# Kernel tuning notes

Measured on AMD Instinct MI355X. Metric: run time of the kernel, lower is better.

Reference implementation:

```python
import jax, jax.numpy as jnp
import numpy as np
from jax import lax

NEGINF = -100000.0
START_IDX = 0  # y_codebook['__START__']
TAGSET = 16


def setup_inputs() -> dict:
    key = jax.random.key(0)
    ks = jax.random.split(key, 8)
    D, H, K, T = 1024, 1024, TAGSET, 8192
    seq = jax.random.normal(ks[0], (1, T, D), dtype=jnp.float32)
    # PyTorch-layout LSTM params: gates ordered (i, f, g, o)
    s = 1.0 / np.sqrt(H)
    W_ih = jax.random.uniform(ks[1], (4 * H, D), jnp.float32, -s, s)
    W_hh = jax.random.uniform(ks[2], (4 * H, H), jnp.float32, -s, s)
    b_ih = jax.random.uniform(ks[3], (4 * H,), jnp.float32, -s, s)
    b_hh = jax.random.uniform(ks[4], (4 * H,), jnp.float32, -s, s)
    W_tag = jax.random.uniform(ks[5], (K, H), jnp.float32, -s, s)
    b_tag = jax.random.uniform(ks[6], (K,), jnp.float32, -s, s)
    trans = jax.random.normal(ks[7], (K, K), dtype=jnp.float32)
    trans = trans.at[:, START_IDX].set(NEGINF)  # nothing transitions INTO start
    return {"seq": seq, "W_ih": W_ih, "W_hh": W_hh, "b_ih": b_ih,
            "b_hh": b_hh, "W_tag": W_tag, "b_tag": b_tag, "trans": trans}


def _lstm(x, W_ih, W_hh, b_ih, b_hh):
    # x: (T, D) -> hidden states (T, H); PyTorch gate order i,f,g,o
    H = W_hh.shape[1]
    x_gates = x @ W_ih.T + (b_ih + b_hh)  # (T, 4H) precomputed input part

    def step(carry, gx):
        h, c = carry
        g = gx + h @ W_hh.T
        i, f, gg, o = jnp.split(g, 4)
        i, f, o = jax.nn.sigmoid(i), jax.nn.sigmoid(f), jax.nn.sigmoid(o)
        c = f * c + i * jnp.tanh(gg)
        h = o * jnp.tanh(c)
        return (h, c), h

    init = (jnp.zeros((H,), x.dtype), jnp.zeros((H,), x.dtype))
    _, hs = lax.scan(step, init, x_gates)
    return hs  # (T, H)


def reference(seq, W_ih, W_hh, b_ih, b_hh, W_tag, b_tag, trans):
    # --- compute_potential (batch=1) ---
    x = seq[0]                                  # (T, D)
    rnnout = _lstm(x, W_ih, W_hh, b_ih, b_hh)    # (T, H)
    feat = rnnout @ W_tag.T + b_tag              # (T, K) unary potentials

    # --- compute_forward_vec: alpha recursion in log-semiring ---
    # feat_score[t, i, j] = feat[t, j] + trans[i, j]
    feat_score = feat[:, None, :] + trans[None, :, :]  # (T, K, K)
    K = trans.shape[0]
    alpha0 = jnp.full((K,), NEGINF, dtype=feat.dtype).at[START_IDX].set(0.0)

    def step(a, fs):
        a_new = jax.nn.logsumexp(a[:, None] + fs, axis=0)  # (K,)
        return a_new, a_new

    a_T, rows = lax.scan(step, alpha0, feat_score)
    alpha = jnp.concatenate([alpha0[None, :], rows], axis=0)  # (T+1, K)
    Z = jax.nn.logsumexp(a_T)  # log partition (no stop state)
    return Z, alpha
```

## Files before the change

### kernel.cpp

```cpp
#include <hip/hip_runtime.h>
#include <hip/hip_bf16.h>
#include <math.h>

#define T_LEN   8192
#define D_IN    1024
#define H_DIM   1024
#define G4      4096
#define K_TAG   16
#define NWG     128
#define NPAIR   512
#define NC      128
#define CLEN    64
#define NEGINF_V (-100000.0f)

__device__ __forceinline__ float fsig(float x) {
  return __fdividef(1.f, 1.f + __expf(-x));
}
__device__ __forceinline__ float ftanh(float x) {
  float e = __expf(fminf(fmaxf(2.f * x, -88.f), 88.f));
  return __fdividef(e - 1.f, e + 1.f);
}

__global__ void k_init(const float* __restrict__ b_ih, const float* __restrict__ b_hh,
                       float* __restrict__ bsum, float* __restrict__ h0,
                       unsigned long long* __restrict__ htag) {
  int tid = blockIdx.x * 256 + threadIdx.x;
  if (tid < G4) bsum[tid] = b_ih[tid] + b_hh[tid];
  if (tid < H_DIM) h0[tid] = 0.f;
  if (tid < 2 * NPAIR) htag[tid] = 0ULL;
}

__global__ __launch_bounds__(256) void k_gemm_xg(
    const float* __restrict__ A,
    const float* __restrict__ B,
    const float* __restrict__ bsum,
    __hip_bfloat16* __restrict__ xg)
{
  __shared__ __align__(16) float As[16][132];
  __shared__ __align__(16) float Bs[16][132];
  const int tid = threadIdx.x;
  const int n0 = blockIdx.x * 128;
  const int m0 = blockIdx.y * 128;
  const int ty = tid >> 4, tx = tid & 15;
  float acc[8][8] = {};

  for (int k0 = 0; k0 < D_IN; k0 += 16) {
#pragma unroll
    for (int p0 = 0; p0 < 2; ++p0) {
      int p = tid + p0 * 256;
      int row = p >> 2;
      int c4 = (p & 3) * 4;
      float4 va = *(const float4*)&A[(size_t)(m0 + row) * D_IN + k0 + c4];
      As[c4 + 0][row] = va.x; As[c4 + 1][row] = va.y;
      As[c4 + 2][row] = va.z; As[c4 + 3][row] = va.w;
      float4 vb = *(const float4*)&B[(size_t)(n0 + row) * D_IN + k0 + c4];
      Bs[c4 + 0][row] = vb.x; Bs[c4 + 1][row] = vb.y;
      Bs[c4 + 2][row] = vb.z; Bs[c4 + 3][row] = vb.w;
    }
    __syncthreads();
#pragma unroll
    for (int k = 0; k < 16; ++k) {
      float4 a0 = *(const float4*)&As[k][ty * 8];
      float4 a1 = *(const float4*)&As[k][ty * 8 + 4];
      float4 b0 = *(const float4*)&Bs[k][tx * 8];
      float4 b1 = *(const float4*)&Bs[k][tx * 8 + 4];
      float av[8] = {a0.x, a0.y, a0.z, a0.w, a1.x, a1.y, a1.z, a1.w};
      float bv[8] = {b0.x, b0.y, b0.z, b0.w, b1.x, b1.y, b1.z, b1.w};
#pragma unroll
      for (int i = 0; i < 8; ++i)
#pragma unroll
        for (int j = 0; j < 8; ++j)
          acc[i][j] = fmaf(av[i], bv[j], acc[i][j]);
    }
    __syncthreads();
  }

#pragma unroll
  for (int i = 0; i < 8; ++i) {
    size_t m = (size_t)(m0 + ty * 8 + i);
    union { __hip_bfloat16 h[8]; uint4 v; } pk;
#pragma unroll
    for (int j = 0; j < 8; ++j)
      pk.h[j] = __float2bfloat16(acc[i][j] + bsum[n0 + tx * 8 + j]);
    *(uint4*)&xg[m * G4 + n0 + tx * 8] = pk.v;
  }
}

__global__ __launch_bounds__(256) void k_lstm(
    const float* __restrict__ W_hh,
    const __hip_bfloat16* __restrict__ xg,
    float* __restrict__ h_all,
    unsigned long long* __restrict__ htag)
{
  __shared__ __align__(16) float h_lds[H_DIM];
  __shared__ unsigned long long hxs[4];

  const int tid = threadIdx.x;
  const int w = blockIdx.x;
  const int lane = tid & 63;
  const int v = tid >> 6;
  const int rl8 = lane >> 3;
  const int sub = lane & 7;
  const int g = rl8 >> 1, b = rl8 & 1;
  const int j = 2 * v + b;
  const int grow = g * H_DIM + w * 8 + j;

  float4 w4[32];
#pragma unroll
  for (int k = 0; k < 32; ++k)
    w4[k] = *(const float4*)&W_hh[(size_t)grow * H_DIM + sub * 4 + 32 * k];

  if (tid < 4) hxs[tid] = 0ULL;
  __syncthreads();

  float c_reg = 0.f;

  for (int t = 1; t <= T_LEN; ++t) {
    float xgv = __bfloat162float(xg[(size_t)(t - 1) * G4 + grow]);

    if (v == 0) {
      unsigned long long* hb = htag + (((t - 1) & 1) << 9);
      const unsigned tgt = (unsigned)(t - 1);
      unsigned long long x0, x1, x2, x3, x4, x5, x6, x7;
      for (;;) {
        x0 = __hip_atomic_load(hb + lane,       __ATOMIC_RELAXED, __HIP_MEMORY_SCOPE_AGENT);
        x1 = __hip_atomic_load(hb + lane + 64,  __ATOMIC_RELAXED, __HIP_MEMORY_SCOPE_AGENT);
        x2 = __hip_atomic_load(hb + lane + 128, __ATOMIC_RELAXED, __HIP_MEMORY_SCOPE_AGENT);
        x3 = __hip_atomic_load(hb + lane + 192, __ATOMIC_RELAXED, __HIP_MEMORY_SCOPE_AGENT);
        x4 = __hip_atomic_load(hb + lane + 256, __ATOMIC_RELAXED, __HIP_MEMORY_SCOPE_AGENT);
        x5 = __hip_atomic_load(hb + lane + 320, __ATOMIC_RELAXED, __HIP_MEMORY_SCOPE_AGENT);
        x6 = __hip_atomic_load(hb + lane + 384, __ATOMIC_RELAXED, __HIP_MEMORY_SCOPE_AGENT);
        x7 = __hip_atomic_load(hb + lane + 448, __ATOMIC_RELAXED, __HIP_MEMORY_SCOPE_AGENT);
        unsigned mn = min(min(min((unsigned)(x0 >> 32), (unsigned)(x1 >> 32)),
                              min((unsigned)(x2 >> 32), (unsigned)(x3 >> 32))),
                          min(min((unsigned)(x4 >> 32), (unsigned)(x5 >> 32)),
                              min((unsigned)(x6 >> 32), (unsigned)(x7 >> 32))));
        if (mn >= tgt) break;
        __builtin_amdgcn_s_sleep(1);
      }
      unsigned long long xs[8] = {x0, x1, x2, x3, x4, x5, x6, x7};
#pragma unroll
      for (int i = 0; i < 8; ++i) {
        unsigned lo = (unsigned)xs[i];
        unsigned short s0 = (unsigned short)lo;
        unsigned short s1 = (unsigned short)(lo >> 16);
        float2 p;
        p.x = __bfloat162float(*(const __hip_bfloat16*)&s0);
        p.y = __bfloat162float(*(const __hip_bfloat16*)&s1);
        ((float2*)h_lds)[lane + 64 * i] = p;
      }
    }
    __syncthreads();

    const float4* h4 = (const float4*)h_lds;
    float acc = 0.f;
#pragma unroll
    for (int k = 0; k < 32; ++k) {
      float4 hv = h4[sub + 8 * k];
      acc = fmaf(w4[k].x, hv.x, acc);
      acc = fmaf(w4[k].y, hv.y, acc);
      acc = fmaf(w4[k].z, hv.z, acc);
      acc = fmaf(w4[k].w, hv.w, acc);
    }
    acc += __shfl_xor(acc, 1);
    acc += __shfl_xor(acc, 2);
    acc += __shfl_xor(acc, 4);
    acc += xgv;

    const int bl = lane & 8;
    float gi = __shfl(acc, bl);
    float gf = __shfl(acc, bl | 16);
    float gg = __shfl(acc, bl | 32);
    float go = __shfl(acc, bl | 48);

    float si = fsig(gi);
    float sf = fsig(gf);
    float so = fsig(go);
    c_reg = sf * c_reg + si * ftanh(gg);
    float h = so * ftanh(c_reg);
    float h_other = __shfl(h, lane ^ 8);

    if (lane == 0) {
      __hip_bfloat16 hb0 = __float2bfloat16(h);
      __hip_bfloat16 hb1 = __float2bfloat16(h_other);
      unsigned lo = (unsigned)*(unsigned short*)&hb0 |
                    ((unsigned)*(unsigned short*)&hb1 << 16);
      unsigned long long pk = ((unsigned long long)(unsigned)t << 32) |
                              (unsigned long long)lo;
      __hip_atomic_store(&hxs[v], pk, __ATOMIC_RELAXED, __HIP_MEMORY_SCOPE_WORKGROUP);
    }
    if ((lane & 55) == 0) {
      h_all[(size_t)t * H_DIM + w * 8 + j] = h;
    }

    if (v == 0 && lane < 4) {
      unsigned long long pk;
      do {
        pk = __hip_atomic_load(&hxs[lane], __ATOMIC_RELAXED, __HIP_MEMORY_SCOPE_WORKGROUP);
      } while ((unsigned)(pk >> 32) != (unsigned)t);
      __hip_atomic_store(htag + ((t & 1) << 9) + w * 4 + lane, pk,
                         __ATOMIC_RELAXED, __HIP_MEMORY_SCOPE_AGENT);
    }
  }
}

__device__ __forceinline__ float lse16(float v) {
  float m = v;
  m = fmaxf(m, __shfl_xor(m, 1));
  m = fmaxf(m, __shfl_xor(m, 2));
  m = fmaxf(m, __shfl_xor(m, 4));
  m = fmaxf(m, __shfl_xor(m, 8));
  float e = expf(v - m);
  e += __shfl_xor(e, 1);
  e += __shfl_xor(e, 2);
  e += __shfl_xor(e, 4);
  e += __shfl_xor(e, 8);
  return m + logf(e);
}

__global__ __launch_bounds__(256) void k_chunk(
    const float* __restrict__ h_all,
    const float* __restrict__ W_tag, const float* __restrict__ b_tag,
    const float* __restrict__ trans,
    float* __restrict__ featbuf,
    float* __restrict__ Pbuf)
{
  __shared__ float trs[16][17];
  __shared__ float featc[CLEN][16];
  __shared__ __align__(16) float hrow[H_DIM];
  __shared__ float red[16][17];
  __shared__ float Pa[16][17], Pb[16][17];

  const int tid = threadIdx.x;
  const int c = blockIdx.x;
  trs[tid >> 4][tid & 15] = trans[tid];

  const int jj = tid & 15, part = tid >> 4;
  for (int u = 0; u < CLEN; ++u) {
    int s = c * CLEN + 1 + u;
    ((float4*)hrow)[tid] = ((const float4*)(h_all + (size_t)s * H_DIM))[tid];
    __syncthreads();
    const float* wt = W_tag + (size_t)jj * H_DIM + part * 64;
    const float* hp = hrow + part * 64;
    float4 a4 = {0.f, 0.f, 0.f, 0.f};
#pragma unroll
    for (int k2 = 0; k2 < 64; k2 += 4) {
      float4 hv = *(const float4*)(hp + k2);
      float4 wv = *(const float4*)(wt + k2);
      a4.x = fmaf(hv.x, wv.x, a4.x);
      a4.y = fmaf(hv.y, wv.y, a4.y);
      a4.z = fmaf(hv.z, wv.z, a4.z);
      a4.w = fmaf(hv.w, wv.w, a4.w);
    }
    red[jj][part] = (a4.x + a4.y) + (a4.z + a4.w);
    __syncthreads();
    if (tid < 16) {
      float ssum = b_tag[tid];
#pragma unroll
      for (int pp = 0; pp < 16; ++pp) ssum += red[tid][pp];
      featc[u][tid] = ssum;
      featbuf[(size_t)s * K_TAG + tid] = ssum;
    }
    __syncthreads();
  }

  const int i = tid >> 4, j = tid & 15;
  Pa[i][j] = trs[i][j] + featc[0][j];
  __syncthreads();
  float* Pr = &Pa[0][0];
  float* Pw = &Pb[0][0];
  for (int u = 1; u < CLEN; ++u) {
    float fj = featc[u][j];
    float m = -3.0e38f;
#pragma unroll
    for (int k = 0; k < 16; ++k) m = fmaxf(m, Pr[i * 17 + k] + trs[k][j]);
    float e = 0.f;
#pragma unroll
    for (int k = 0; k < 16; ++k) e += expf(Pr[i * 17 + k] + trs[k][j] - m);
    Pw[i * 17 + j] = m + fj + logf(e);
    __syncthreads();
    float* tsw = Pr; Pr = Pw; Pw = tsw;
  }
  Pbuf[(size_t)c * 256 + i * 16 + j] = Pr[i * 17 + j];
}

__global__ __launch_bounds__(256) void k_scan(
    const float* __restrict__ Pbuf,
    float* __restrict__ bbuf,
    float* __restrict__ out)
{
  __shared__ float Pl[16][17];
  __shared__ float bcur[16], bnew[16];
  const int tid = threadIdx.x;
  const int i = tid & 15, j = tid >> 4;
  if (tid < 16) {
    float a0 = (tid == 0) ? 0.f : NEGINF_V;
    bcur[tid] = a0;
    bbuf[tid] = a0;
    out[1 + tid] = a0;
  }
  __syncthreads();
  for (int c = 0; c < NC; ++c) {
    Pl[tid >> 4][tid & 15] = Pbuf[(size_t)c * 256 + tid];
    __syncthreads();
    float r_ = lse16(bcur[i] + Pl[i][j]);
    if (i == 0) bnew[j] = r_;
    __syncthreads();
    if (tid < 16) {
      bcur[tid] = bnew[tid];
      bbuf[(size_t)(c + 1) * K_TAG + tid] = bnew[tid];
    }
    __syncthreads();
  }
  if (tid < 16) {
    float z = lse16(bcur[tid]);
    if (tid == 0) out[0] = z;
  }
}

__global__ __launch_bounds__(256) void k_alpha(
    const float* __restrict__ featbuf, const float* __restrict__ trans,
    const float* __restrict__ bbuf, float* __restrict__ out)
{
  __shared__ float trs[16][17];
  __shared__ float acur[16], anew[16];
  const int tid = threadIdx.x;
  const int c = blockIdx.x;
  trs[tid >> 4][tid & 15] = trans[tid];
  if (tid < 16) acur[tid] = bbuf[(size_t)c * K_TAG + tid];
  __syncthreads();
  const int i = tid & 15, j = tid >> 4;
  for (int u = 0; u < CLEN; ++u) {
    int s = c * CLEN + 1 + u;
    float v = acur[i] + trs[i][j] + featbuf[(size_t)s * K_TAG + j];
    float r_ = lse16(v);
    if (i == 0) anew[j] = r_;
    __syncthreads();
    if (tid < 16) {
      acur[tid] = anew[tid];
      out[1 + (size_t)s * K_TAG + tid] = anew[tid];
    }
    __syncthreads();
  }
}

extern "C" void kernel_launch(void* const* d_in, const int* in_sizes, int n_in,
                              void* d_out, int out_size, void* d_ws, size_t ws_size,
                              hipStream_t stream) {
  (void)in_sizes; (void)n_in; (void)out_size; (void)ws_size;
  const float* seq   = (const float*)d_in[0];
  const float* W_ih  = (const float*)d_in[1];
  const float* W_hh  = (const float*)d_in[2];
  const float* b_ih  = (const float*)d_in[3];
  const float* b_hh  = (const float*)d_in[4];
  const float* W_tag = (const float*)d_in[5];
  const float* b_tag = (const float*)d_in[6];
  const float* trans = (const float*)d_in[7];
  float* out = (float*)d_out;

  char* base = (char*)d_ws;
  size_t off = 0;
  auto take = [&](size_t nbytes) -> void* {
    void* p = base + off;
    off += (nbytes + 255) & ~(size_t)255;
    return p;
  };
  __hip_bfloat16* xg = (__hip_bfloat16*)take((size_t)T_LEN * G4 * sizeof(__hip_bfloat16));
  float* h_all   = (float*)take((size_t)(T_LEN + 1) * H_DIM * sizeof(float));
  float* featbuf = (float*)take((size_t)(T_LEN + 1) * K_TAG * sizeof(float));
  float* Pbuf    = (float*)take((size_t)NC * 256 * sizeof(float));
  float* bbuf    = (float*)take((size_t)(NC + 1) * K_TAG * sizeof(float));
  float* bsum    = (float*)take((size_t)G4 * sizeof(float));
  unsigned long long* htag = (unsigned long long*)take((size_t)2 * NPAIR * sizeof(unsigned long long));

  k_init<<<16, 256, 0, stream>>>(b_ih, b_hh, bsum, h_all, htag);
  k_gemm_xg<<<dim3(G4 / 128, T_LEN / 128), 256, 0, stream>>>(seq, W_ih, bsum, xg);
  k_lstm<<<NWG, 256, 0, stream>>>(W_hh, xg, h_all, htag);
  k_chunk<<<NC, 256, 0, stream>>>(h_all, W_tag, b_tag, trans, featbuf, Pbuf);
  k_scan<<<1, 256, 0, stream>>>(Pbuf, bbuf, out);
  k_alpha<<<NC, 256, 0, stream>>>(featbuf, trans, bbuf, out);
}
```

Before: 20.07 ms.

## Halve persistent LSTM workgroups to 64 with 512 threads and split FMA chains

The persistent recurrent LSTM kernel now runs 64 workgroups of 512 threads, each owning 16 hidden units instead of 8, so fewer workgroups take part in the per-step cross-workgroup flag exchange. The goal is to cut global synchronisation latency per timestep. The dot product also now uses four independent accumulators to shorten the serial FMA dependency chain. In exchange, each workgroup does more work per step, register pressure under the 512-thread launch bound may rise, and only half as many compute units are used.

```diff
diff --git a/kernel.cpp b/kernel.cpp
--- a/kernel.cpp
+++ b/kernel.cpp
@@ -7,7 +7,7 @@
 #define H_DIM   1024
 #define G4      4096
 #define K_TAG   16
-#define NWG     128
+#define NWG     64
 #define NPAIR   512
 #define NC      128
 #define CLEN    64
@@ -86,14 +86,14 @@
   }
 }
 
-__global__ __launch_bounds__(256) void k_lstm(
+__global__ __launch_bounds__(512) void k_lstm(
     const float* __restrict__ W_hh,
     const __hip_bfloat16* __restrict__ xg,
     float* __restrict__ h_all,
     unsigned long long* __restrict__ htag)
 {
   __shared__ __align__(16) float h_lds[H_DIM];
-  __shared__ unsigned long long hxs[4];
+  __shared__ unsigned long long hxs[8];
 
   const int tid = threadIdx.x;
   const int w = blockIdx.x;
@@ -103,14 +103,14 @@
   const int sub = lane & 7;
   const int g = rl8 >> 1, b = rl8 & 1;
   const int j = 2 * v + b;
-  const int grow = g * H_DIM + w * 8 + j;
+  const int grow = g * H_DIM + w * 16 + j;
 
   float4 w4[32];
 #pragma unroll
   for (int k = 0; k < 32; ++k)
     w4[k] = *(const float4*)&W_hh[(size_t)grow * H_DIM + sub * 4 + 32 * k];
 
-  if (tid < 4) hxs[tid] = 0ULL;
+  if (tid < 8) hxs[tid] = 0ULL;
   __syncthreads();
 
   float c_reg = 0.f;
@@ -153,15 +153,31 @@
     __syncthreads();
 
     const float4* h4 = (const float4*)h_lds;
-    float acc = 0.f;
-#pragma unroll
-    for (int k = 0; k < 32; ++k) {
-      float4 hv = h4[sub + 8 * k];
-      acc = fmaf(w4[k].x, hv.x, acc);
-      acc = fmaf(w4[k].y, hv.y, acc);
-      acc = fmaf(w4[k].z, hv.z, acc);
-      acc = fmaf(w4[k].w, hv.w, acc);
-    }
+    float ac0 = 0.f, ac1 = 0.f, ac2 = 0.f, ac3 = 0.f;
+#pragma unroll
+    for (int k = 0; k < 32; k += 4) {
+      float4 hv0 = h4[sub + 8 * k];
+      float4 hv1 = h4[sub + 8 * (k + 1)];
+      float4 hv2 = h4[sub + 8 * (k + 2)];
+      float4 hv3 = h4[sub + 8 * (k + 3)];
+      ac0 = fmaf(w4[k].x, hv0.x, ac0);
+      ac0 = fmaf(w4[k].y, hv0.y, ac0);
+      ac0 = fmaf(w4[k].z, hv0.z, ac0);
+      ac0 = fmaf(w4[k].w, hv0.w, ac0);
+      ac1 = fmaf(w4[k + 1].x, hv1.x, ac1);
+      ac1 = fmaf(w4[k + 1].y, hv1.y, ac1);
+      ac1 = fmaf(w4[k + 1].z, hv1.z, ac1);
+      ac1 = fmaf(w4[k + 1].w, hv1.w, ac1);
+      ac2 = fmaf(w4[k + 2].x, hv2.x, ac2);
+      ac2 = fmaf(w4[k + 2].y, hv2.y, ac2);
+      ac2 = fmaf(w4[k + 2].z, hv2.z, ac2);
+      ac2 = fmaf(w4[k + 2].w, hv2.w, ac2);
+      ac3 = fmaf(w4[k + 3].x, hv3.x, ac3);
+      ac3 = fmaf(w4[k + 3].y, hv3.y, ac3);
+      ac3 = fmaf(w4[k + 3].z, hv3.z, ac3);
+      ac3 = fmaf(w4[k + 3].w, hv3.w, ac3);
+    }
+    float acc = (ac0 + ac1) + (ac2 + ac3);
     acc += __shfl_xor(acc, 1);
     acc += __shfl_xor(acc, 2);
     acc += __shfl_xor(acc, 4);
@@ -190,15 +206,15 @@
       __hip_atomic_store(&hxs[v], pk, __ATOMIC_RELAXED, __HIP_MEMORY_SCOPE_WORKGROUP);
     }
     if ((lane & 55) == 0) {
-      h_all[(size_t)t * H_DIM + w * 8 + j] = h;
-    }
-
-    if (v == 0 && lane < 4) {
+      h_all[(size_t)t * H_DIM + w * 16 + j] = h;
+    }
+
+    if (v == 0 && lane < 8) {
       unsigned long long pk;
       do {
         pk = __hip_atomic_load(&hxs[lane], __ATOMIC_RELAXED, __HIP_MEMORY_SCOPE_WORKGROUP);
       } while ((unsigned)(pk >> 32) != (unsigned)t);
-      __hip_atomic_store(htag + ((t & 1) << 9) + w * 4 + lane, pk,
+      __hip_atomic_store(htag + ((t & 1) << 9) + w * 8 + lane, pk,
                          __ATOMIC_RELAXED, __HIP_MEMORY_SCOPE_AGENT);
     }
   }
@@ -375,7 +391,7 @@
 
   k_init<<<16, 256, 0, stream>>>(b_ih, b_hh, bsum, h_all, htag);
   k_gemm_xg<<<dim3(G4 / 128, T_LEN / 128), 256, 0, stream>>>(seq, W_ih, bsum, xg);
-  k_lstm<<<NWG, 256, 0, stream>>>(W_hh, xg, h_all, htag);
+  k_lstm<<<NWG, 512, 0, stream>>>(W_hh, xg, h_all, htag);
   k_chunk<<<NC, 256, 0, stream>>>(h_all, W_tag, b_tag, trans, featbuf, Pbuf);
   k_scan<<<1, 256, 0, stream>>>(Pbuf, bbuf, out);
   k_alpha<<<NC, 256, 0, stream>>>(featbuf, trans, bbuf, out);
```

After: 19.39 ms, median of 2. -3.4%, faster.
